# Kernel tuning notes

Hardware: AMD Instinct MI355X
Metric: run time of the kernel (lower is better)

Reference implementation:

```python
import jax, jax.numpy as jnp
import numpy as np

NEG_SLOPE = 0.2  # PyG GATConv default negative_slope


def gat_conv(x, edge_index, W, att_src, att_dst, bias, concat):
    """PyG-style GATConv (eval mode, add_self_loops=True).
    W: [in, H*C]; att_src/att_dst: [H, C]; bias: [H*C] or [C]."""
    N = x.shape[0]
    H, C = att_src.shape
    loop = jnp.arange(N, dtype=edge_index.dtype)
    src = jnp.concatenate([edge_index[0], loop])  # message sources
    dst = jnp.concatenate([edge_index[1], loop])  # aggregation targets
    h = (x @ W).reshape(N, H, C)                  # [N, H, C]
    a_s = jnp.einsum('nhc,hc->nh', h, att_src)    # [N, H]
    a_d = jnp.einsum('nhc,hc->nh', h, att_dst)
    e = jax.nn.leaky_relu(a_s[src] + a_d[dst], NEG_SLOPE)  # [E, H]
    # segment softmax over incoming edges of each destination node
    m = jax.ops.segment_max(e, dst, num_segments=N)
    ex = jnp.exp(e - m[dst])
    denom = jax.ops.segment_sum(ex, dst, num_segments=N)
    alpha = ex / (denom[dst] + 1e-16)             # [E, H]
    out = jax.ops.segment_sum(h[src] * alpha[:, :, None], dst, num_segments=N)
    out = out.reshape(N, H * C) if concat else out.mean(axis=1)
    return out + bias


def setup_inputs() -> dict:
    key = jax.random.key(0)
    ks = jax.random.split(key, 13)
    N, E, G = 100000, 3200000, 512
    IN, HID, HEADS, OUT = 1, 8, 8, 10
    p = lambda k, shape: jax.random.normal(k, shape, jnp.float32) * 0.1
    return {
        'x': jax.random.normal(ks[0], (N, IN), jnp.float32),
        'edge_index': jax.random.randint(ks[1], (2, E), 0, N),
        'batch': jnp.sort(jax.random.randint(ks[2], (N,), 0, G)),
        'num_graphs': G,
        'W1': p(ks[3], (IN, HEADS * HID)),
        'att_src1': p(ks[4], (HEADS, HID)),
        'att_dst1': p(ks[5], (HEADS, HID)),
        'b1': jnp.zeros((HEADS * HID,), jnp.float32),
        'W2': p(ks[6], (HEADS * HID, HID)),
        'att_src2': p(ks[7], (1, HID)),
        'att_dst2': p(ks[8], (1, HID)),
        'b2': jnp.zeros((HID,), jnp.float32),
        'lin_w': p(ks[9], (HID, OUT)),
        'lin_b': jnp.zeros((OUT,), jnp.float32),
    }


def reference(x, edge_index, batch, num_graphs, W1, att_src1, att_dst1, b1,
              W2, att_src2, att_dst2, b2, lin_w, lin_b):
    # eval mode: F.dropout is identity
    h = gat_conv(x, edge_index, W1, att_src1, att_dst1, b1, concat=True)   # [N, 64]
    h = jax.nn.elu(h)
    h = gat_conv(h, edge_index, W2, att_src2, att_dst2, b2, concat=False)  # [N, 8]
    # global mean pool over graphs
    sums = jax.ops.segment_sum(h, batch, num_segments=num_graphs)
    cnt = jax.ops.segment_sum(jnp.ones((h.shape[0], 1), h.dtype), batch,
                              num_segments=num_graphs)
    pooled = sums / jnp.maximum(cnt, 1.0)                                   # [G, 8]
    logits = pooled @ lin_w + lin_b                                         # [G, 10]
    return jax.nn.log_softmax(logits, axis=1)
```

## Files before the change

kernel.cpp:

```cpp
#include <hip/hip_runtime.h>
#include <hip/hip_bf16.h>

#define HEADS 8
#define HID 8
#define NEG 0.2f

#define NBMAX 512
#define BCAP 12288
#define TILE 8192

__global__ void __launch_bounds__(512) kP_bucket(
    const int* __restrict__ src, const int* __restrict__ dst,
    int* __restrict__ gcur, unsigned int* __restrict__ packed, int E, int NB)
{
    __shared__ int hist[NBMAX], lofs[NBMAX], gbase[NBMAX], cur[NBMAX], s[NBMAX];
    __shared__ unsigned int stage[TILE];
    int tid = threadIdx.x;
    hist[tid] = 0;
    __syncthreads();
    int t0 = blockIdx.x * TILE;
    int tend = t0 + TILE; if (tend > E) tend = E;
    for (int i = t0 + tid; i < tend; i += 512)
        atomicAdd(&hist[dst[i] >> 8], 1);
    __syncthreads();
    int v = hist[tid];
    s[tid] = v;
    __syncthreads();
    for (int off = 1; off < NBMAX; off <<= 1) {
        int t = (tid >= off) ? s[tid - off] : 0;
        __syncthreads();
        s[tid] += t;
        __syncthreads();
    }
    lofs[tid] = s[tid] - v;
    gbase[tid] = v ? atomicAdd(&gcur[tid], v) : 0;
    cur[tid] = 0;
    __syncthreads();
    for (int i = t0 + tid; i < tend; i += 512) {
        int d = dst[i];
        int j = d >> 8;
        int pos = lofs[j] + atomicAdd(&cur[j], 1);
        stage[pos] = ((unsigned)src[i] << 8) | (unsigned)(d & 255);
    }
    __syncthreads();
    int wave = tid >> 6, lane = tid & 63;
    for (int j = wave; j < NB; j += 8) {
        int h = hist[j], lo = lofs[j], gb = gbase[j];
        for (int k = lane; k < h; k += 64) {
            int gp = gb + k;
            if (gp < BCAP) packed[(size_t)j * BCAP + gp] = stage[lo + k];
        }
    }
}

__global__ void __launch_bounds__(256) kF_fine(
    const int* __restrict__ gcur, unsigned int* packed,
    int* __restrict__ rowS, int* __restrict__ rowE, int N)
{
    __shared__ int hist[256], roff[256], cur[256];
    __shared__ int stage[BCAP];
    int b = blockIdx.x;
    size_t base = (size_t)b * BCAP;
    int cnt = gcur[b]; if (cnt > BCAP) cnt = BCAP;
    int tid = threadIdx.x;
    hist[tid] = 0;
    __syncthreads();
    for (int i = tid; i < cnt; i += 256)
        atomicAdd(&hist[packed[base + i] & 255], 1);
    __syncthreads();
    int v = hist[tid];
    roff[tid] = v;
    __syncthreads();
    for (int off = 1; off < 256; off <<= 1) {
        int t = (tid >= off) ? roff[tid - off] : 0;
        __syncthreads();
        roff[tid] += t;
        __syncthreads();
    }
    int excl = roff[tid] - v;
    cur[tid] = excl;
    int node = b * 256 + tid;
    if (node < N) { rowS[node] = (int)base + excl; rowE[node] = (int)base + excl + v; }
    __syncthreads();
    for (int i = tid; i < cnt; i += 256) {
        unsigned p = packed[base + i];
        int pos = atomicAdd(&cur[p & 255], 1);
        stage[pos] = (int)(p >> 8);
    }
    __syncthreads();
    for (int i = tid; i < cnt; i += 256)
        packed[base + i] = (unsigned)stage[i];
}

__global__ void __launch_bounds__(256) kG1_gather(
    const int* __restrict__ rowS, const int* __restrict__ rowE,
    const unsigned int* __restrict__ csr,
    const float* __restrict__ x,
    const float* __restrict__ W1, const float* __restrict__ as1, const float* __restrict__ ad1,
    float* __restrict__ num1, float* __restrict__ den1, int N)
{
    __shared__ float S1[HEADS], D1[HEADS];
    if (threadIdx.x < HEADS) {
        float s = 0.f, d = 0.f;
        for (int c = 0; c < HID; ++c) {
            float w = W1[threadIdx.x * HID + c];
            s += w * as1[threadIdx.x * HID + c];
            d += w * ad1[threadIdx.x * HID + c];
        }
        S1[threadIdx.x] = s; D1[threadIdx.x] = d;
    }
    __syncthreads();
    int t = blockIdx.x * blockDim.x + threadIdx.x;
    int node = t >> 3, lane = t & 7;
    if (node >= N) return;
    float xdv = x[node];
    float den[8] = {0,0,0,0,0,0,0,0}, num[8] = {0,0,0,0,0,0,0,0};
    if (lane == 0) {
        #pragma unroll
        for (int h = 0; h < 8; ++h) {
            float e = xdv * (S1[h] + D1[h]);
            e = fmaxf(e, NEG * e);
            float w = __expf(e);
            den[h] = w; num[h] = w * xdv;
        }
    }
    int start = rowS[node], end = rowE[node];
    for (int j = start + lane; j < end; j += 8) {
        int s = (int)csr[j];
        float xsv = x[s];
        #pragma unroll
        for (int h = 0; h < 8; ++h) {
            float e = xsv * S1[h] + xdv * D1[h];
            e = fmaxf(e, NEG * e);
            float w = __expf(e);
            den[h] += w; num[h] += w * xsv;
        }
    }
    #pragma unroll
    for (int off = 4; off >= 1; off >>= 1) {
        #pragma unroll
        for (int h = 0; h < 8; ++h) {
            den[h] += __shfl_down(den[h], off, 8);
            num[h] += __shfl_down(num[h], off, 8);
        }
    }
    if (lane == 0) {
        #pragma unroll
        for (int h = 0; h < 8; ++h) {
            num1[node * 8 + h] = num[h];
            den1[node * 8 + h] = den[h];
        }
    }
}

__global__ void __launch_bounds__(256) k3_node_mid(
    const float* __restrict__ num1, const float* __restrict__ den1,
    const float* __restrict__ W1, const float* __restrict__ b1,
    const float* __restrict__ W2,
    const float* __restrict__ as2w, const float* __restrict__ ad2w,
    float* __restrict__ h2, float* __restrict__ as2, float* __restrict__ ad2, int N)
{
    __shared__ float sW1[64], sb1[64], sW2[512], sas[8], sad[8];
    for (int i = threadIdx.x; i < 64; i += blockDim.x) { sW1[i] = W1[i]; sb1[i] = b1[i]; }
    for (int i = threadIdx.x; i < 512; i += blockDim.x) sW2[i] = W2[i];
    if (threadIdx.x < 8) { sas[threadIdx.x] = as2w[threadIdx.x]; sad[threadIdx.x] = ad2w[threadIdx.x]; }
    __syncthreads();
    int n = blockIdx.x * blockDim.x + threadIdx.x;
    if (n >= N) return;
    float h1[64];
    #pragma unroll
    for (int h = 0; h < 8; ++h) {
        float agg = num1[n * 8 + h] / (den1[n * 8 + h] + 1e-16f);
        #pragma unroll
        for (int c = 0; c < 8; ++c) {
            float v = agg * sW1[h * 8 + c] + sb1[h * 8 + c];
            h1[h * 8 + c] = v > 0.f ? v : (__expf(v) - 1.f);
        }
    }
    float o[8] = {0,0,0,0,0,0,0,0};
    #pragma unroll
    for (int k = 0; k < 64; ++k) {
        float hv = h1[k];
        #pragma unroll
        for (int c = 0; c < 8; ++c) o[c] += hv * sW2[k * 8 + c];
    }
    float as_ = 0.f, ad_ = 0.f;
    #pragma unroll
    for (int c = 0; c < 8; ++c) {
        as_ += o[c] * sas[c];
        ad_ += o[c] * sad[c];
        h2[(size_t)n * 8 + c] = o[c];
    }
    as2[n] = as_; ad2[n] = ad_;
}

__global__ void __launch_bounds__(256) kG2_gather(
    const int* __restrict__ rowS, const int* __restrict__ rowE,
    const unsigned int* __restrict__ csr,
    const float* __restrict__ as2, const float* __restrict__ ad2,
    const float* __restrict__ h2,
    float* __restrict__ out2, int N)
{
    int t = blockIdx.x * blockDim.x + threadIdx.x;
    int node = t >> 3, lane = t & 7;
    if (node >= N) return;
    float add = ad2[node];
    float den = 0.f, num[8] = {0,0,0,0,0,0,0,0};
    if (lane == 0) {
        float e = as2[node] + add;
        e = fmaxf(e, NEG * e);
        float w = __expf(e);
        den = w;
        const float4* hp = (const float4*)&h2[(size_t)node * 8];
        float4 a = hp[0], b = hp[1];
        num[0] = w * a.x; num[1] = w * a.y; num[2] = w * a.z; num[3] = w * a.w;
        num[4] = w * b.x; num[5] = w * b.y; num[6] = w * b.z; num[7] = w * b.w;
    }
    int start = rowS[node], end = rowE[node];
    for (int j = start + lane; j < end; j += 8) {
        int s = (int)csr[j];
        float e = as2[s] + add;
        e = fmaxf(e, NEG * e);
        float w = __expf(e);
        den += w;
        const float4* hp = (const float4*)&h2[(size_t)s * 8];
        float4 a = hp[0], b = hp[1];
        num[0] += w * a.x; num[1] += w * a.y; num[2] += w * a.z; num[3] += w * a.w;
        num[4] += w * b.x; num[5] += w * b.y; num[6] += w * b.z; num[7] += w * b.w;
    }
    #pragma unroll
    for (int off = 4; off >= 1; off >>= 1) {
        den += __shfl_down(den, off, 8);
        #pragma unroll
        for (int c = 0; c < 8; ++c) num[c] += __shfl_down(num[c], off, 8);
    }
    if (lane == 0) {
        float dv = den + 1e-16f;
        #pragma unroll
        for (int c = 0; c < 8; ++c) out2[(size_t)node * 8 + c] = num[c] / dv;
    }
}

__global__ void __launch_bounds__(256) kB_starts(
    const int* __restrict__ batch, int* __restrict__ gstart, int N, int G)
{
    int n = blockIdx.x * blockDim.x + threadIdx.x;
    if (n >= N) return;
    int b0 = batch[n];
    if (n == 0) {
        for (int g = 0; g <= b0; ++g) gstart[g] = 0;
    } else {
        int bp = batch[n - 1];
        for (int g = bp + 1; g <= b0; ++g) gstart[g] = n;
    }
    if (n == N - 1) {
        for (int g = b0 + 1; g <= G; ++g) gstart[g] = N;
    }
}

__global__ void __launch_bounds__(256) kPool(
    const float* __restrict__ out2, const int* __restrict__ gstart,
    const float* __restrict__ b2v,
    const float* __restrict__ lin_w, const float* __restrict__ lin_b,
    float* __restrict__ out, int G)
{
    __shared__ float sw[80], sb[10], sb2[8];
    if (threadIdx.x < 80) sw[threadIdx.x] = lin_w[threadIdx.x];
    if (threadIdx.x < 10) sb[threadIdx.x] = lin_b[threadIdx.x];
    if (threadIdx.x < 8)  sb2[threadIdx.x] = b2v[threadIdx.x];
    __syncthreads();
    int wid = (blockIdx.x * blockDim.x + threadIdx.x) >> 6;
    if (wid >= G) return;
    int lane = threadIdx.x & 63;
    int ch = lane & 7, sub = lane >> 3;
    int start = gstart[wid], end = gstart[wid + 1];
    int cntn = end - start;
    float acc = 0.f;
    for (int i = start + sub; i < end; i += 8)
        acc += out2[(size_t)i * 8 + ch];
    acc += __shfl_down(acc, 32, 64);
    acc += __shfl_down(acc, 16, 64);
    acc += __shfl_down(acc, 8, 64);
    float inv = (cntn > 0) ? 1.f / (float)cntn : 0.f;
    float p[8];
    #pragma unroll
    for (int i = 0; i < 8; ++i) {
        float tt = __shfl(acc, i, 64);
        p[i] = (cntn > 0) ? (tt * inv + sb2[i]) : 0.f;
    }
    float l[10]; float m = -1e30f;
    #pragma unroll
    for (int j = 0; j < 10; ++j) {
        float v = sb[j];
        #pragma unroll
        for (int i = 0; i < 8; ++i) v += p[i] * sw[i * 10 + j];
        l[j] = v; m = v > m ? v : m;
    }
    float sum = 0.f;
    #pragma unroll
    for (int j = 0; j < 10; ++j) sum += __expf(l[j] - m);
    float lse = m + __logf(sum);
    if (lane < 10) out[(size_t)wid * 10 + lane] = l[lane] - lse;
}

extern "C" void kernel_launch(void* const* d_in, const int* in_sizes, int n_in,
                              void* d_out, int out_size, void* d_ws, size_t ws_size,
                              hipStream_t stream) {
    const float* x    = (const float*)d_in[0];
    const int*   ei   = (const int*)d_in[1];
    const int*   batch= (const int*)d_in[2];
    const float* W1   = (const float*)d_in[4];
    const float* as1  = (const float*)d_in[5];
    const float* ad1  = (const float*)d_in[6];
    const float* b1   = (const float*)d_in[7];
    const float* W2   = (const float*)d_in[8];
    const float* as2w = (const float*)d_in[9];
    const float* ad2w = (const float*)d_in[10];
    const float* b2v  = (const float*)d_in[11];
    const float* lw   = (const float*)d_in[12];
    const float* lb   = (const float*)d_in[13];
    float* out = (float*)d_out;

    const int N = in_sizes[0];
    const int E = in_sizes[1] / 2;
    const int G = out_size / 10;
    const int* srcI = ei;
    const int* dstI = ei + E;
    const int NB = (N + 255) >> 8;

    int*   gcur = (int*)d_ws;
    unsigned int* packed = (unsigned int*)(gcur + 512);
    int*   rowS = (int*)(packed + (size_t)NB * BCAP);
    int*   rowE = rowS + N;
    float* num1 = (float*)(rowE + N);
    float* den1 = num1 + (size_t)8 * N;
    float* h2   = den1 + (size_t)8 * N;
    float* as2  = h2 + (size_t)8 * N;
    float* ad2  = as2 + N;
    float* out2 = ad2 + N;
    int*   gstart = (int*)(out2 + (size_t)8 * N);

    const int B = 256;
    hipMemsetAsync(gcur, 0, 512 * sizeof(int), stream);

    kP_bucket<<<(E + TILE - 1) / TILE, 512, 0, stream>>>(srcI, dstI, gcur, packed, E, NB);
    kB_starts<<<(N + B - 1) / B, B, 0, stream>>>(batch, gstart, N, G);
    kF_fine<<<NB, B, 0, stream>>>(gcur, packed, rowS, rowE, N);
    kG1_gather<<<(N * 8 + B - 1) / B, B, 0, stream>>>(rowS, rowE, packed, x,
                                                      W1, as1, ad1, num1, den1, N);
    k3_node_mid<<<(N + B - 1) / B, B, 0, stream>>>(num1, den1, W1, b1, W2, as2w, ad2w,
                                                   h2, as2, ad2, N);
    kG2_gather<<<(N * 8 + B - 1) / B, B, 0, stream>>>(rowS, rowE, packed, as2, ad2, h2,
                                                      out2, N);
    kPool<<<(G * 64 + B - 1) / B, B, 0, stream>>>(out2, gstart, b2v, lw, lb, out, G);
}
```

Before: 230.1 us.

## Fuse CSR fine sort, layer-1 gather and node transform into one kernel

Merges the per-bucket fine sort, the layer-1 attention gather and the per-node mid transform into one 512-thread kernel per 256-node bucket. The layer-1 gather reads source indices straight from the shared-memory staging buffer and keeps num/den in registers, so the num1/den1 round trip and two launches go away. In exchange, parallelism per node drops from 8 lanes to 2 and only 391 blocks run. Those blocks hold about 50KB of LDS each, which may leave the GPU underused and lengthen per-node edge loops.

```diff
diff --git a/kernel.cpp b/kernel.cpp
--- a/kernel.cpp
+++ b/kernel.cpp
@@ -1,10 +1,7 @@
 #include <hip/hip_runtime.h>
 #include <hip/hip_bf16.h>
 
-#define HEADS 8
-#define HID 8
 #define NEG 0.2f
-
 #define NBMAX 512
 #define BCAP 12288
 #define TILE 8192
@@ -53,145 +50,113 @@
     }
 }
 
-__global__ void __launch_bounds__(256) kF_fine(
+__global__ void __launch_bounds__(512) kL1(
     const int* __restrict__ gcur, unsigned int* packed,
-    int* __restrict__ rowS, int* __restrict__ rowE, int N)
+    const float* __restrict__ x,
+    const float* __restrict__ W1, const float* __restrict__ as1, const float* __restrict__ ad1,
+    const float* __restrict__ b1, const float* __restrict__ W2,
+    const float* __restrict__ as2w, const float* __restrict__ ad2w,
+    int* __restrict__ rowS, int* __restrict__ rowE,
+    float* __restrict__ h2, float* __restrict__ as2, float* __restrict__ ad2, int N)
 {
     __shared__ int hist[256], roff[256], cur[256];
     __shared__ int stage[BCAP];
-    int b = blockIdx.x;
+    __shared__ float S1[8], D1[8], sW1[64], sb1[64], sW2[512], sas[8], sad[8];
+    int tid = threadIdx.x, b = blockIdx.x;
+    if (tid < 8) {
+        float sv = 0.f, dv = 0.f;
+        for (int c = 0; c < 8; ++c) {
+            float w = W1[tid * 8 + c];
+            sv += w * as1[tid * 8 + c];
+            dv += w * ad1[tid * 8 + c];
+        }
+        S1[tid] = sv; D1[tid] = dv;
+        sas[tid] = as2w[tid]; sad[tid] = ad2w[tid];
+    }
+    for (int i = tid; i < 64; i += 512) { sW1[i] = W1[i]; sb1[i] = b1[i]; }
+    if (tid < 512) sW2[tid] = W2[tid];
+    if (tid < 256) hist[tid] = 0;
+    __syncthreads();
+    int cnt = gcur[b]; if (cnt > BCAP) cnt = BCAP;
     size_t base = (size_t)b * BCAP;
-    int cnt = gcur[b]; if (cnt > BCAP) cnt = BCAP;
-    int tid = threadIdx.x;
-    hist[tid] = 0;
-    __syncthreads();
-    for (int i = tid; i < cnt; i += 256)
-        atomicAdd(&hist[packed[base + i] & 255], 1);
-    __syncthreads();
-    int v = hist[tid];
-    roff[tid] = v;
+    unsigned int* pk = packed + base;
+    for (int i = tid; i < cnt; i += 512)
+        atomicAdd(&hist[pk[i] & 255], 1);
+    __syncthreads();
+    int v = (tid < 256) ? hist[tid] : 0;
+    if (tid < 256) roff[tid] = v;
     __syncthreads();
     for (int off = 1; off < 256; off <<= 1) {
-        int t = (tid >= off) ? roff[tid - off] : 0;
+        int t = (tid >= off && tid < 256) ? roff[tid - off] : 0;
         __syncthreads();
-        roff[tid] += t;
+        if (tid < 256) roff[tid] += t;
         __syncthreads();
     }
-    int excl = roff[tid] - v;
-    cur[tid] = excl;
-    int node = b * 256 + tid;
-    if (node < N) { rowS[node] = (int)base + excl; rowE[node] = (int)base + excl + v; }
-    __syncthreads();
-    for (int i = tid; i < cnt; i += 256) {
-        unsigned p = packed[base + i];
+    if (tid < 256) cur[tid] = roff[tid] - v;
+    __syncthreads();
+    for (int i = tid; i < cnt; i += 512) {
+        unsigned p = pk[i];
         int pos = atomicAdd(&cur[p & 255], 1);
         stage[pos] = (int)(p >> 8);
     }
     __syncthreads();
-    for (int i = tid; i < cnt; i += 256)
-        packed[base + i] = (unsigned)stage[i];
-}
-
-__global__ void __launch_bounds__(256) kG1_gather(
-    const int* __restrict__ rowS, const int* __restrict__ rowE,
-    const unsigned int* __restrict__ csr,
-    const float* __restrict__ x,
-    const float* __restrict__ W1, const float* __restrict__ as1, const float* __restrict__ ad1,
-    float* __restrict__ num1, float* __restrict__ den1, int N)
-{
-    __shared__ float S1[HEADS], D1[HEADS];
-    if (threadIdx.x < HEADS) {
-        float s = 0.f, d = 0.f;
-        for (int c = 0; c < HID; ++c) {
-            float w = W1[threadIdx.x * HID + c];
-            s += w * as1[threadIdx.x * HID + c];
-            d += w * ad1[threadIdx.x * HID + c];
-        }
-        S1[threadIdx.x] = s; D1[threadIdx.x] = d;
-    }
-    __syncthreads();
-    int t = blockIdx.x * blockDim.x + threadIdx.x;
-    int node = t >> 3, lane = t & 7;
-    if (node >= N) return;
-    float xdv = x[node];
-    float den[8] = {0,0,0,0,0,0,0,0}, num[8] = {0,0,0,0,0,0,0,0};
-    if (lane == 0) {
+    for (int i = tid; i < cnt; i += 512)
+        pk[i] = (unsigned)stage[i];
+    int nl = tid >> 1, sub = tid & 1;
+    int node = b * 256 + nl;
+    bool valid = node < N;
+    int end = roff[nl], start = end - hist[nl];
+    if (valid && sub == 0) { rowS[node] = (int)base + start; rowE[node] = (int)base + end; }
+    float xdv = valid ? x[node] : 0.f;
+    float s1r[8], d1r[8];
+    #pragma unroll
+    for (int h = 0; h < 8; ++h) { s1r[h] = S1[h]; d1r[h] = D1[h]; }
+    float num[8] = {0,0,0,0,0,0,0,0}, den[8] = {0,0,0,0,0,0,0,0};
+    if (valid && sub == 0) {
         #pragma unroll
         for (int h = 0; h < 8; ++h) {
-            float e = xdv * (S1[h] + D1[h]);
+            float e = xdv * (s1r[h] + d1r[h]);
             e = fmaxf(e, NEG * e);
             float w = __expf(e);
             den[h] = w; num[h] = w * xdv;
         }
     }
-    int start = rowS[node], end = rowE[node];
-    for (int j = start + lane; j < end; j += 8) {
-        int s = (int)csr[j];
-        float xsv = x[s];
+    for (int j = start + sub; j < end; j += 2) {
+        float xsv = x[stage[j]];
         #pragma unroll
         for (int h = 0; h < 8; ++h) {
-            float e = xsv * S1[h] + xdv * D1[h];
+            float e = xsv * s1r[h] + xdv * d1r[h];
             e = fmaxf(e, NEG * e);
             float w = __expf(e);
             den[h] += w; num[h] += w * xsv;
         }
     }
     #pragma unroll
-    for (int off = 4; off >= 1; off >>= 1) {
-        #pragma unroll
-        for (int h = 0; h < 8; ++h) {
-            den[h] += __shfl_down(den[h], off, 8);
-            num[h] += __shfl_down(num[h], off, 8);
-        }
-    }
-    if (lane == 0) {
-        #pragma unroll
-        for (int h = 0; h < 8; ++h) {
-            num1[node * 8 + h] = num[h];
-            den1[node * 8 + h] = den[h];
-        }
-    }
-}
-
-__global__ void __launch_bounds__(256) k3_node_mid(
-    const float* __restrict__ num1, const float* __restrict__ den1,
-    const float* __restrict__ W1, const float* __restrict__ b1,
-    const float* __restrict__ W2,
-    const float* __restrict__ as2w, const float* __restrict__ ad2w,
-    float* __restrict__ h2, float* __restrict__ as2, float* __restrict__ ad2, int N)
-{
-    __shared__ float sW1[64], sb1[64], sW2[512], sas[8], sad[8];
-    for (int i = threadIdx.x; i < 64; i += blockDim.x) { sW1[i] = W1[i]; sb1[i] = b1[i]; }
-    for (int i = threadIdx.x; i < 512; i += blockDim.x) sW2[i] = W2[i];
-    if (threadIdx.x < 8) { sas[threadIdx.x] = as2w[threadIdx.x]; sad[threadIdx.x] = ad2w[threadIdx.x]; }
-    __syncthreads();
-    int n = blockIdx.x * blockDim.x + threadIdx.x;
-    if (n >= N) return;
-    float h1[64];
-    #pragma unroll
     for (int h = 0; h < 8; ++h) {
-        float agg = num1[n * 8 + h] / (den1[n * 8 + h] + 1e-16f);
+        den[h] += __shfl_xor(den[h], 1, 64);
+        num[h] += __shfl_xor(num[h], 1, 64);
+    }
+    if (!valid || sub) return;
+    float o[8] = {0,0,0,0,0,0,0,0};
+    #pragma unroll
+    for (int h = 0; h < 8; ++h) {
+        float agg = num[h] / (den[h] + 1e-16f);
         #pragma unroll
         for (int c = 0; c < 8; ++c) {
-            float v = agg * sW1[h * 8 + c] + sb1[h * 8 + c];
-            h1[h * 8 + c] = v > 0.f ? v : (__expf(v) - 1.f);
-        }
-    }
-    float o[8] = {0,0,0,0,0,0,0,0};
-    #pragma unroll
-    for (int k = 0; k < 64; ++k) {
-        float hv = h1[k];
-        #pragma unroll
-        for (int c = 0; c < 8; ++c) o[c] += hv * sW2[k * 8 + c];
+            float vv = agg * sW1[h * 8 + c] + sb1[h * 8 + c];
+            vv = vv > 0.f ? vv : (__expf(vv) - 1.f);
+            #pragma unroll
+            for (int c2 = 0; c2 < 8; ++c2) o[c2] += vv * sW2[(h * 8 + c) * 8 + c2];
+        }
     }
     float as_ = 0.f, ad_ = 0.f;
     #pragma unroll
     for (int c = 0; c < 8; ++c) {
         as_ += o[c] * sas[c];
         ad_ += o[c] * sad[c];
-        h2[(size_t)n * 8 + c] = o[c];
-    }
-    as2[n] = as_; ad2[n] = ad_;
+        h2[(size_t)node * 8 + c] = o[c];
+    }
+    as2[node] = as_; ad2[node] = ad_;
 }
 
 __global__ void __launch_bounds__(256) kG2_gather(
@@ -332,9 +297,7 @@
     unsigned int* packed = (unsigned int*)(gcur + 512);
     int*   rowS = (int*)(packed + (size_t)NB * BCAP);
     int*   rowE = rowS + N;
-    float* num1 = (float*)(rowE + N);
-    float* den1 = num1 + (size_t)8 * N;
-    float* h2   = den1 + (size_t)8 * N;
+    float* h2   = (float*)(rowE + N);
     float* as2  = h2 + (size_t)8 * N;
     float* ad2  = as2 + N;
     float* out2 = ad2 + N;
@@ -345,11 +308,8 @@
 
     kP_bucket<<<(E + TILE - 1) / TILE, 512, 0, stream>>>(srcI, dstI, gcur, packed, E, NB);
     kB_starts<<<(N + B - 1) / B, B, 0, stream>>>(batch, gstart, N, G);
-    kF_fine<<<NB, B, 0, stream>>>(gcur, packed, rowS, rowE, N);
-    kG1_gather<<<(N * 8 + B - 1) / B, B, 0, stream>>>(rowS, rowE, packed, x,
-                                                      W1, as1, ad1, num1, den1, N);
-    k3_node_mid<<<(N + B - 1) / B, B, 0, stream>>>(num1, den1, W1, b1, W2, as2w, ad2w,
-                                                   h2, as2, ad2, N);
+    kL1<<<NB, 512, 0, stream>>>(gcur, packed, x, W1, as1, ad1, b1, W2, as2w, ad2w,
+                                rowS, rowE, h2, as2, ad2, N);
     kG2_gather<<<(N * 8 + B - 1) / B, B, 0, stream>>>(rowS, rowE, packed, as2, ad2, h2,
                                                       out2, N);
     kPool<<<(G * 64 + B - 1) / B, B, 0, stream>>>(out2, gstart, b2v, lw, lb, out, G);
```

Result: faster. 213.9 us (-7.0%).
